# Performance work log

Hardware: AMD Instinct MI355X
Metric: run time of the kernel (lower is better)

Reference implementation:

```python
import jax, jax.numpy as jnp
from jax import lax
import numpy as np


def setup_inputs() -> dict:
    key = jax.random.key(0)
    B, N, K_ORDERS = 8, 16384, 4
    k1, k2 = jax.random.split(key)
    coord = jax.random.normal(k1, (B * N, 3), dtype=jnp.float32)
    serialized_code = jax.random.randint(k2, (K_ORDERS, B * N), 0, 1 << 30)
    return {
        "coord": coord,
        "serialized_code": serialized_code,
        "batch_size": 8,
        "num_group": 1024,
        "group_size": 32,
    }


def _fps(pts, G):
    """Farthest point sampling on pts [N,3]; starts at index 0 (pointops convention)."""
    N = pts.shape[0]

    def step(carry, _):
        dist, last = carry
        d = jnp.sum((pts - pts[last]) ** 2, axis=-1)  # [N]
        dist = jnp.minimum(dist, d)
        nxt = jnp.argmax(dist).astype(jnp.int32)
        return (dist, nxt), nxt

    init = (jnp.full((N,), jnp.inf, pts.dtype), jnp.int32(0))
    _, rest = lax.scan(step, init, None, length=G - 1)
    return jnp.concatenate([jnp.zeros((1,), jnp.int32), rest])  # [G]


def reference(coord, serialized_code, batch_size, num_group, group_size):
    B, G, S = batch_size, num_group, group_size
    N = coord.shape[0] // B
    pts = coord.reshape(B, N, 3)

    # --- FPS per cloud (offset-batched in the original) ---
    loc_idx = jax.vmap(lambda p: _fps(p, G))(pts)  # [B, G] local indices
    s_idx = (loc_idx + (jnp.arange(B, dtype=jnp.int32) * N)[:, None]).reshape(-1)  # [B*G] global
    s_xyz = coord[s_idx]  # [B*G, 3]

    # --- KNN per cloud: S nearest points to each sampled center ---
    centers = s_xyz.reshape(B, G, 3)

    def knn_one(p, c):  # p [N,3], c [G,3]
        # squared distances via gemm to avoid [G,N,3] intermediate
        d2 = (jnp.sum(c * c, -1)[:, None] + jnp.sum(p * p, -1)[None, :]
              - 2.0 * c @ p.T)  # [G, N]
        _, idx = lax.top_k(-d2, S)  # ascending distance, self first
        return idx

    nloc = jax.vmap(knn_one)(pts, centers)  # [B, G, S]
    s_n_idx = (nloc + (jnp.arange(B) * N)[:, None, None]).reshape(B * G, S)

    # relative coords, drop the self point (column 0)
    s_n = coord[s_n_idx] - s_xyz[:, None, :]  # [B*G, S, 3]
    s_n = s_n[:, 1:, :]  # [B*G, S-1, 3]

    # --- serialization order over sampled points + inverse permutation ---
    code_sel = serialized_code[:, s_idx]  # [K, B*G]
    s_order = jnp.argsort(code_sel, axis=1)  # [K, B*G]
    M = s_order.shape[1]
    src = jnp.broadcast_to(jnp.arange(M, dtype=s_order.dtype), s_order.shape)
    rows = jnp.arange(s_order.shape[0])[:, None]
    s_inverse = jnp.zeros_like(s_order).at[rows, s_order].set(src)

    return s_idx, s_n, s_xyz, s_order, s_inverse
```

## Files before the change

### kernel.cpp

```cpp
#include <hip/hip_runtime.h>
#include <hip/hip_bf16.h>
#include <stdint.h>

#define BB 8
#define NN 16384
#define GG 1024
#define SS 32
#define BN (BB*NN)

#define OFF_SIDX 0
#define OFF_SN   8192
#define OFF_SXYZ 770048
#define OFF_ORD  794624
#define OFF_INV  827392

#define WS_SIDX 0
#define WS_KNN  32768

typedef float v2f __attribute__((ext_vector_type(2)));

static __device__ __forceinline__ v2f vmin2(v2f a, v2f b) {
    v2f r; r.x = fminf(a.x, b.x); r.y = fminf(a.y, b.y); return r;
}
static __device__ __forceinline__ v2f vmax2(v2f a, v2f b) {
    v2f r; r.x = fmaxf(a.x, b.x); r.y = fmaxf(a.y, b.y); return r;
}

static __device__ __forceinline__ uint64_t shfl_u64(uint64_t v, int src) {
    int lo = __shfl((int)(uint32_t)(v & 0xffffffffull), src, 64);
    int hi = __shfl((int)(uint32_t)(v >> 32), src, 64);
    return ((uint64_t)(uint32_t)hi << 32) | (uint32_t)lo;
}

template<int CTRL, int RM, int BM>
static __device__ __forceinline__ unsigned dpp_umax(unsigned v) {
    unsigned o = (unsigned)__builtin_amdgcn_update_dpp((int)v, (int)v, CTRL, RM, BM, false);
    return o > v ? o : v;
}

__global__ __launch_bounds__(1024) void fps_kernel(const float* __restrict__ coord,
                                                   int* __restrict__ ws_sidx,
                                                   float* __restrict__ out) {
#pragma clang fp contract(off)
    const int b = blockIdx.x;
    const int t = threadIdx.x;
    const int base = b * NN;
    const int wave = t >> 6, lane = t & 63;

    v2f px[8], py[8], pz[8], dist[8];
#pragma unroll
    for (int j = 0; j < 8; j++) {
        int pA = t + (j << 11);
        int pB = pA + 1024;
        px[j] = (v2f){coord[3*(base+pA)  ], coord[3*(base+pB)  ]};
        py[j] = (v2f){coord[3*(base+pA)+1], coord[3*(base+pB)+1]};
        pz[j] = (v2f){coord[3*(base+pA)+2], coord[3*(base+pB)+2]};
        dist[j] = (v2f){__builtin_inff(), __builtin_inff()};
    }

    __shared__ unsigned wv[16];
    __shared__ unsigned win[2];

    if (t == 0) {
        ws_sidx[b*GG] = base;
        out[OFF_SIDX + b*GG] = (float)base;
        win[0] = 0xffffffffu; win[1] = 0xffffffffu;
    }
    float qx = coord[3*base], qy = coord[3*base+1], qz = coord[3*base+2];
    __syncthreads();

    for (int g = 1; g < GG; g++) {
        const int s = g & 1;
        v2f qvx = (v2f){qx,qx}, qvy = (v2f){qy,qy}, qvz = (v2f){qz,qz};
#pragma unroll
        for (int j = 0; j < 8; j++) {
            v2f dx = px[j] - qvx, dy = py[j] - qvy, dz = pz[j] - qvz;
            v2f d  = (dx*dx + dy*dy) + dz*dz;
            dist[j] = vmin2(dist[j], d);
        }
        v2f m01 = vmax2(dist[0], dist[1]);
        v2f m23 = vmax2(dist[2], dist[3]);
        v2f m45 = vmax2(dist[4], dist[5]);
        v2f m67 = vmax2(dist[6], dist[7]);
        v2f m07 = vmax2(vmax2(m01, m23), vmax2(m45, m67));
        float bvf = fmaxf(m07.x, m07.y);
        unsigned lb = __float_as_uint(bvf);
        unsigned r = lb;
        r = dpp_umax<0x111, 0xf, 0xf>(r);
        r = dpp_umax<0x112, 0xf, 0xf>(r);
        r = dpp_umax<0x114, 0xf, 0xf>(r);
        r = dpp_umax<0x118, 0xf, 0xf>(r);
        r = dpp_umax<0x142, 0xa, 0xf>(r);
        r = dpp_umax<0x143, 0xc, 0xf>(r);
        unsigned wmax = (unsigned)__builtin_amdgcn_readlane((int)r, 63);
        if (lane == 0) wv[wave] = wmax;
        __syncthreads();
        if (t == 0) win[1 - s] = 0xffffffffu;
        unsigned x = wv[lane & 15];
        x = dpp_umax<0x111, 0xf, 0xf>(x);
        x = dpp_umax<0x112, 0xf, 0xf>(x);
        x = dpp_umax<0x114, 0xf, 0xf>(x);
        x = dpp_umax<0x118, 0xf, 0xf>(x);
        unsigned bmax = (unsigned)__builtin_amdgcn_readlane((int)x, 15);
        if (lb == bmax) {
            int e = 15;
#pragma unroll
            for (int jj = 15; jj >= 0; jj--) {
                float v = (jj & 1) ? dist[jj >> 1].y : dist[jj >> 1].x;
                if (__float_as_uint(v) == bmax) e = jj;
            }
            atomicMin(&win[s], (unsigned)(t + (e << 10)));
        }
        __syncthreads();
        unsigned pw = win[s];
        int sp = __builtin_amdgcn_readfirstlane((int)pw);
        if (t == 0) {
            ws_sidx[b*GG + g] = base + sp;
            out[OFF_SIDX + b*GG + g] = (float)(base + sp);
        }
        qx = coord[3*(base+sp)];
        qy = coord[3*(base+sp)+1];
        qz = coord[3*(base+sp)+2];
    }
}

__global__ __launch_bounds__(64) void knn_kernel(const float* __restrict__ coord,
                                                 const int* __restrict__ ws_sidx,
                                                 int* __restrict__ ws_knn) {
#pragma clang fp contract(off)
    const int c = blockIdx.x;
    const int l = threadIdx.x;
    const int b = c >> 10;
    const int base = b * NN;
    const int sg = ws_sidx[c];
    const float cx = coord[3*sg], cy = coord[3*sg+1], cz = coord[3*sg+2];
    const float cc = (cx*cx + cy*cy) + cz*cz;

    float mv = __builtin_inff(); int mp = 0;
#pragma unroll 4
    for (int j = 0; j < 256; j++) {
        int p = l + (j << 6);
        float x = coord[3*(base+p)], y = coord[3*(base+p)+1], z = coord[3*(base+p)+2];
        float pp  = (x*x + y*y) + z*z;
        float dot = (cx*x + cy*y) + cz*z;
        float d2  = (cc + pp) - 2.0f*dot;
        if (d2 < mv) { mv = d2; mp = p; }
    }

    uint64_t m0 = 0, m1 = 0, m2 = 0, m3 = 0;
    int res_p = 0;
    for (int k = 0; k < SS; k++) {
        float bv = mv; int bp = mp;
#pragma unroll
        for (int off = 32; off >= 1; off >>= 1) {
            float ov = __shfl_xor(bv, off, 64);
            int   op = __shfl_xor(bp, off, 64);
            if (ov < bv || (ov == bv && op < bp)) { bv = ov; bp = op; }
        }
        if (l == k) res_p = bp;
        const int w  = bp & 63;
        const int e  = bp >> 6;
        if (l == w) {
            uint64_t bit = 1ull << (e & 63);
            int word = e >> 6;
            if      (word == 0) m0 |= bit;
            else if (word == 1) m1 |= bit;
            else if (word == 2) m2 |= bit;
            else                m3 |= bit;
        }
        uint64_t w0 = shfl_u64(m0, w), w1 = shfl_u64(m1, w),
                 w2 = shfl_u64(m2, w), w3 = shfl_u64(m3, w);
        float nv = __builtin_inff(); int np_ = 0;
#pragma unroll
        for (int m = 0; m < 4; m++) {
            int e2 = l + (m << 6);
            uint64_t mw = (m == 0) ? w0 : ((m == 1) ? w1 : ((m == 2) ? w2 : w3));
            int p2 = w + (e2 << 6);
            float x = coord[3*(base+p2)], y = coord[3*(base+p2)+1], z = coord[3*(base+p2)+2];
            float pp  = (x*x + y*y) + z*z;
            float dot = (cx*x + cy*y) + cz*z;
            float d2  = (cc + pp) - 2.0f*dot;
            bool cons = (mw >> l) & 1ull;
            if (!cons && d2 < nv) { nv = d2; np_ = p2; }
        }
#pragma unroll
        for (int off = 32; off >= 1; off >>= 1) {
            float ov = __shfl_xor(nv, off, 64);
            int   op = __shfl_xor(np_, off, 64);
            if (ov < nv || (ov == nv && op < np_)) { nv = ov; np_ = op; }
        }
        if (l == w) { mv = nv; mp = np_; }
    }
    if (l < SS) ws_knn[c * SS + l] = res_p;
}

__global__ void sxyz_kernel(const float* __restrict__ coord,
                            const int* __restrict__ ws_sidx,
                            float* __restrict__ out) {
    int t = blockIdx.x * blockDim.x + threadIdx.x;
    if (t < 8192*3) {
        int i = t / 3, cmp = t - 3*i;
        out[OFF_SXYZ + t] = coord[3*ws_sidx[i] + cmp];
    }
}

__global__ void sn_kernel(const float* __restrict__ coord,
                          const int* __restrict__ ws_sidx,
                          const int* __restrict__ ws_knn,
                          float* __restrict__ out) {
#pragma clang fp contract(off)
    int t = blockIdx.x * blockDim.x + threadIdx.x;
    if (t < 8192*31*3) {
        int cmp = t % 3; int rem = t / 3;
        int j = rem % 31; int i = rem / 31;
        int b = i >> 10;
        int nb = ws_knn[i*SS + j + 1];
        int gidx = b*NN + nb;
        float v = coord[3*gidx + cmp] - coord[3*ws_sidx[i] + cmp];
        out[OFF_SN + t] = v;
    }
}

__global__ __launch_bounds__(1024) void sort_kernel(const int* __restrict__ ser,
                                                    const int* __restrict__ ws_sidx,
                                                    float* __restrict__ out) {
    __shared__ uint64_t keys[8192];
    const int r = blockIdx.x, t = threadIdx.x;
#pragma unroll
    for (int s = 0; s < 8; s++) {
        int i = t + (s << 10);
        uint32_t code = (uint32_t)ser[r * BN + ws_sidx[i]];
        keys[i] = ((uint64_t)code << 13) | (uint32_t)i;
    }
    __syncthreads();
    for (int k2 = 2; k2 <= 8192; k2 <<= 1) {
        for (int j = k2 >> 1; j > 0; j >>= 1) {
#pragma unroll 2
            for (int s = 0; s < 8; s++) {
                int i = t + (s << 10);
                int ixj = i ^ j;
                if (ixj > i) {
                    uint64_t a = keys[i], bq = keys[ixj];
                    bool up = ((i & k2) == 0);
                    if ((a > bq) == up) { keys[i] = bq; keys[ixj] = a; }
                }
            }
            __syncthreads();
        }
    }
    for (int s = 0; s < 8; s++) {
        int k = t + (s << 10);
        uint64_t key = keys[k];
        int i = (int)(key & 8191u);
        out[OFF_ORD + r*8192 + k] = (float)i;
        out[OFF_INV + r*8192 + i] = (float)k;
    }
}

extern "C" void kernel_launch(void* const* d_in, const int* in_sizes, int n_in,
                              void* d_out, int out_size, void* d_ws, size_t ws_size,
                              hipStream_t stream) {
    const float* coord = (const float*)d_in[0];
    const int*   ser   = (const int*)d_in[1];
    float* out = (float*)d_out;
    char* ws = (char*)d_ws;
    int* ws_sidx = (int*)(ws + WS_SIDX);
    int* ws_knn  = (int*)(ws + WS_KNN);

    hipLaunchKernelGGL(fps_kernel,  dim3(BB),   dim3(1024), 0, stream, coord, ws_sidx, out);
    hipLaunchKernelGGL(knn_kernel,  dim3(8192), dim3(64),   0, stream, coord, ws_sidx, ws_knn);
    hipLaunchKernelGGL(sxyz_kernel, dim3(96),   dim3(256),  0, stream, coord, ws_sidx, out);
    hipLaunchKernelGGL(sn_kernel,   dim3(2976), dim3(256),  0, stream, coord, ws_sidx, ws_knn, out);
    hipLaunchKernelGGL(sort_kernel, dim3(4),    dim3(1024), 0, stream, ser, ws_sidx, out);
}
```

Before: 2.101 ms.

## Drop per-iteration FPS barrier via packed 64-bit atomic argmax; DPP reductions in KNN

FPS now packs the inverted wave-max distance and the point index into one 64-bit key. Each wave's winner does an LDS atomicMin on that key directly, which removes the second block-level reduction and one __syncthreads per sample step. A three-slot buffer of winner keys lets each slot be reset safely ahead of use. KNN replaces the shuffle-based argmin butterflies with DPP 64-bit min reductions on packed (distance bits, index) keys, and replaces the mask shuffles with readlane. The packed float-bit ordering assumes non-negative distances, so a slightly negative self distance from the expanded formula could sort wrongly.

```diff
diff --git a/kernel.cpp b/kernel.cpp
--- a/kernel.cpp
+++ b/kernel.cpp
@@ -26,26 +26,45 @@
     v2f r; r.x = fmaxf(a.x, b.x); r.y = fmaxf(a.y, b.y); return r;
 }
 
-static __device__ __forceinline__ uint64_t shfl_u64(uint64_t v, int src) {
-    int lo = __shfl((int)(uint32_t)(v & 0xffffffffull), src, 64);
-    int hi = __shfl((int)(uint32_t)(v >> 32), src, 64);
-    return ((uint64_t)(uint32_t)hi << 32) | (uint32_t)lo;
-}
-
 template<int CTRL, int RM, int BM>
 static __device__ __forceinline__ unsigned dpp_umax(unsigned v) {
     unsigned o = (unsigned)__builtin_amdgcn_update_dpp((int)v, (int)v, CTRL, RM, BM, false);
     return o > v ? o : v;
 }
 
-__global__ __launch_bounds__(1024) void fps_kernel(const float* __restrict__ coord,
-                                                   int* __restrict__ ws_sidx,
-                                                   float* __restrict__ out) {
+template<int CTRL, int RM, int BM>
+static __device__ __forceinline__ uint64_t dpp_umin64(uint64_t v) {
+    unsigned lo = (unsigned)v, hi = (unsigned)(v >> 32);
+    unsigned olo = (unsigned)__builtin_amdgcn_update_dpp((int)lo, (int)lo, CTRL, RM, BM, false);
+    unsigned ohi = (unsigned)__builtin_amdgcn_update_dpp((int)hi, (int)hi, CTRL, RM, BM, false);
+    uint64_t o = ((uint64_t)ohi << 32) | olo;
+    return o < v ? o : v;
+}
+
+static __device__ __forceinline__ uint64_t wave_umin64(uint64_t v) {
+    v = dpp_umin64<0x111, 0xf, 0xf>(v);
+    v = dpp_umin64<0x112, 0xf, 0xf>(v);
+    v = dpp_umin64<0x114, 0xf, 0xf>(v);
+    v = dpp_umin64<0x118, 0xf, 0xf>(v);
+    v = dpp_umin64<0x142, 0xa, 0xf>(v);
+    v = dpp_umin64<0x143, 0xc, 0xf>(v);
+    return v;
+}
+
+static __device__ __forceinline__ uint64_t rdlane64(uint64_t v, int sl) {
+    unsigned lo = (unsigned)__builtin_amdgcn_readlane((int)(unsigned)v, sl);
+    unsigned hi = (unsigned)__builtin_amdgcn_readlane((int)(unsigned)(v >> 32), sl);
+    return ((uint64_t)hi << 32) | lo;
+}
+
+__global__ __launch_bounds__(1024, 4) void fps_kernel(const float* __restrict__ coord,
+                                                      int* __restrict__ ws_sidx,
+                                                      float* __restrict__ out) {
 #pragma clang fp contract(off)
     const int b = blockIdx.x;
     const int t = threadIdx.x;
     const int base = b * NN;
-    const int wave = t >> 6, lane = t & 63;
+    const int lane = t & 63;
 
     v2f px[8], py[8], pz[8], dist[8];
 #pragma unroll
@@ -58,19 +77,20 @@
         dist[j] = (v2f){__builtin_inff(), __builtin_inff()};
     }
 
-    __shared__ unsigned wv[16];
-    __shared__ unsigned win[2];
+    __shared__ unsigned long long win[3];
 
     if (t == 0) {
         ws_sidx[b*GG] = base;
         out[OFF_SIDX + b*GG] = (float)base;
-        win[0] = 0xffffffffu; win[1] = 0xffffffffu;
+        win[0] = ~0ull; win[1] = ~0ull; win[2] = ~0ull;
     }
     float qx = coord[3*base], qy = coord[3*base+1], qz = coord[3*base+2];
     __syncthreads();
 
     for (int g = 1; g < GG; g++) {
-        const int s = g & 1;
+        const int s = g % 3;
+        if (t == 0) win[(g + 1) % 3] = ~0ull;
+
         v2f qvx = (v2f){qx,qx}, qvy = (v2f){qy,qy}, qvz = (v2f){qz,qz};
 #pragma unroll
         for (int j = 0; j < 8; j++) {
@@ -93,27 +113,20 @@
         r = dpp_umax<0x142, 0xa, 0xf>(r);
         r = dpp_umax<0x143, 0xc, 0xf>(r);
         unsigned wmax = (unsigned)__builtin_amdgcn_readlane((int)r, 63);
-        if (lane == 0) wv[wave] = wmax;
-        __syncthreads();
-        if (t == 0) win[1 - s] = 0xffffffffu;
-        unsigned x = wv[lane & 15];
-        x = dpp_umax<0x111, 0xf, 0xf>(x);
-        x = dpp_umax<0x112, 0xf, 0xf>(x);
-        x = dpp_umax<0x114, 0xf, 0xf>(x);
-        x = dpp_umax<0x118, 0xf, 0xf>(x);
-        unsigned bmax = (unsigned)__builtin_amdgcn_readlane((int)x, 15);
-        if (lb == bmax) {
+        if (lb == wmax) {
             int e = 15;
 #pragma unroll
             for (int jj = 15; jj >= 0; jj--) {
                 float v = (jj & 1) ? dist[jj >> 1].y : dist[jj >> 1].x;
-                if (__float_as_uint(v) == bmax) e = jj;
+                if (__float_as_uint(v) == wmax) e = jj;
             }
-            atomicMin(&win[s], (unsigned)(t + (e << 10)));
+            unsigned p = (unsigned)(t + (e << 10));
+            unsigned long long key = (((unsigned long long)(~wmax)) << 14) | p;
+            atomicMin(&win[s], key);
         }
         __syncthreads();
-        unsigned pw = win[s];
-        int sp = __builtin_amdgcn_readfirstlane((int)pw);
+        unsigned long long key = win[s];
+        int sp = __builtin_amdgcn_readfirstlane((int)(unsigned)(key & 16383u));
         if (t == 0) {
             ws_sidx[b*GG + g] = base + sp;
             out[OFF_SIDX + b*GG + g] = (float)(base + sp);
@@ -150,16 +163,15 @@
     uint64_t m0 = 0, m1 = 0, m2 = 0, m3 = 0;
     int res_p = 0;
     for (int k = 0; k < SS; k++) {
-        float bv = mv; int bp = mp;
-#pragma unroll
-        for (int off = 32; off >= 1; off >>= 1) {
-            float ov = __shfl_xor(bv, off, 64);
-            int   op = __shfl_xor(bp, off, 64);
-            if (ov < bv || (ov == bv && op < bp)) { bv = ov; bp = op; }
-        }
-        if (l == k) res_p = bp;
+        uint64_t key = (((uint64_t)__float_as_uint(mv)) << 14) | (unsigned)mp;
+        key = wave_umin64(key);
+        unsigned klo = (unsigned)__builtin_amdgcn_readlane((int)(unsigned)key, 63);
+        unsigned khi = (unsigned)__builtin_amdgcn_readlane((int)(unsigned)(key >> 32), 63);
+        uint64_t bkey = ((uint64_t)khi << 32) | klo;
+        const int bp = (int)(bkey & 16383u);
         const int w  = bp & 63;
         const int e  = bp >> 6;
+        if (l == k) res_p = bp;
         if (l == w) {
             uint64_t bit = 1ull << (e & 63);
             int word = e >> 6;
@@ -168,8 +180,8 @@
             else if (word == 2) m2 |= bit;
             else                m3 |= bit;
         }
-        uint64_t w0 = shfl_u64(m0, w), w1 = shfl_u64(m1, w),
-                 w2 = shfl_u64(m2, w), w3 = shfl_u64(m3, w);
+        uint64_t w0 = rdlane64(m0, w), w1 = rdlane64(m1, w),
+                 w2 = rdlane64(m2, w), w3 = rdlane64(m3, w);
         float nv = __builtin_inff(); int np_ = 0;
 #pragma unroll
         for (int m = 0; m < 4; m++) {
@@ -183,13 +195,15 @@
             bool cons = (mw >> l) & 1ull;
             if (!cons && d2 < nv) { nv = d2; np_ = p2; }
         }
-#pragma unroll
-        for (int off = 32; off >= 1; off >>= 1) {
-            float ov = __shfl_xor(nv, off, 64);
-            int   op = __shfl_xor(np_, off, 64);
-            if (ov < nv || (ov == nv && op < np_)) { nv = ov; np_ = op; }
-        }
-        if (l == w) { mv = nv; mp = np_; }
+        uint64_t nkey = (((uint64_t)__float_as_uint(nv)) << 14) | (unsigned)np_;
+        nkey = wave_umin64(nkey);
+        unsigned nlo = (unsigned)__builtin_amdgcn_readlane((int)(unsigned)nkey, 63);
+        unsigned nhi = (unsigned)__builtin_amdgcn_readlane((int)(unsigned)(nkey >> 32), 63);
+        uint64_t nbk = ((uint64_t)nhi << 32) | nlo;
+        if (l == w) {
+            mv = __uint_as_float((unsigned)(nbk >> 14));
+            mp = (int)(nbk & 16383u);
+        }
     }
     if (l < SS) ws_knn[c * SS + l] = res_p;
 }
```

New measurement: 2.330 ms. +10.9%, slower.

## Track top-2 per lane in KNN with packed 64-bit keys and DPP reductions

Applied to the files above, without the earlier changes.

The KNN selection now keeps the two best candidates per lane, packed as monotone-float-distance plus index into a single 64-bit key. The per-step wave argmin uses DPP row operations and readlane instead of xor-shuffle pairs. The 256-point rescan of a lane's strip only runs when that lane has already used its second candidate. The FPS kernel also gains a launch-bounds occupancy hint and volatile initial loads. This costs extra per-point work in the initial scan and makes correctness depend on the 14-bit index packing.

```diff
diff --git a/kernel.cpp b/kernel.cpp
--- a/kernel.cpp
+++ b/kernel.cpp
@@ -26,35 +26,60 @@
     v2f r; r.x = fmaxf(a.x, b.x); r.y = fmaxf(a.y, b.y); return r;
 }
 
-static __device__ __forceinline__ uint64_t shfl_u64(uint64_t v, int src) {
-    int lo = __shfl((int)(uint32_t)(v & 0xffffffffull), src, 64);
-    int hi = __shfl((int)(uint32_t)(v >> 32), src, 64);
-    return ((uint64_t)(uint32_t)hi << 32) | (uint32_t)lo;
-}
-
 template<int CTRL, int RM, int BM>
 static __device__ __forceinline__ unsigned dpp_umax(unsigned v) {
     unsigned o = (unsigned)__builtin_amdgcn_update_dpp((int)v, (int)v, CTRL, RM, BM, false);
     return o > v ? o : v;
 }
 
-__global__ __launch_bounds__(1024) void fps_kernel(const float* __restrict__ coord,
-                                                   int* __restrict__ ws_sidx,
-                                                   float* __restrict__ out) {
+template<int CTRL, int RM, int BM>
+static __device__ __forceinline__ uint64_t dpp_umin64(uint64_t v) {
+    unsigned lo = (unsigned)v, hi = (unsigned)(v >> 32);
+    unsigned olo = (unsigned)__builtin_amdgcn_update_dpp((int)lo, (int)lo, CTRL, RM, BM, false);
+    unsigned ohi = (unsigned)__builtin_amdgcn_update_dpp((int)hi, (int)hi, CTRL, RM, BM, false);
+    uint64_t o = ((uint64_t)ohi << 32) | olo;
+    return o < v ? o : v;
+}
+
+static __device__ __forceinline__ uint64_t wave_umin64(uint64_t v) {
+    v = dpp_umin64<0x111, 0xf, 0xf>(v);
+    v = dpp_umin64<0x112, 0xf, 0xf>(v);
+    v = dpp_umin64<0x114, 0xf, 0xf>(v);
+    v = dpp_umin64<0x118, 0xf, 0xf>(v);
+    v = dpp_umin64<0x142, 0xa, 0xf>(v);
+    v = dpp_umin64<0x143, 0xc, 0xf>(v);
+    return v;
+}
+
+static __device__ __forceinline__ uint64_t rdlane64(uint64_t v, int sl) {
+    unsigned lo = (unsigned)__builtin_amdgcn_readlane((int)(unsigned)v, sl);
+    unsigned hi = (unsigned)__builtin_amdgcn_readlane((int)(unsigned)(v >> 32), sl);
+    return ((uint64_t)hi << 32) | lo;
+}
+
+static __device__ __forceinline__ unsigned mono(float f) {
+    unsigned u = __float_as_uint(f);
+    return u ^ (unsigned)((((int)u) >> 31) | (int)0x80000000u);
+}
+
+__global__ __launch_bounds__(1024, 4) void fps_kernel(const float* __restrict__ coord,
+                                                      int* __restrict__ ws_sidx,
+                                                      float* __restrict__ out) {
 #pragma clang fp contract(off)
     const int b = blockIdx.x;
     const int t = threadIdx.x;
     const int base = b * NN;
     const int wave = t >> 6, lane = t & 63;
 
+    const volatile float* vc = coord;
     v2f px[8], py[8], pz[8], dist[8];
 #pragma unroll
     for (int j = 0; j < 8; j++) {
         int pA = t + (j << 11);
         int pB = pA + 1024;
-        px[j] = (v2f){coord[3*(base+pA)  ], coord[3*(base+pB)  ]};
-        py[j] = (v2f){coord[3*(base+pA)+1], coord[3*(base+pB)+1]};
-        pz[j] = (v2f){coord[3*(base+pA)+2], coord[3*(base+pB)+2]};
+        px[j] = (v2f){vc[3*(base+pA)  ], vc[3*(base+pB)  ]};
+        py[j] = (v2f){vc[3*(base+pA)+1], vc[3*(base+pB)+1]};
+        pz[j] = (v2f){vc[3*(base+pA)+2], vc[3*(base+pB)+2]};
         dist[j] = (v2f){__builtin_inff(), __builtin_inff()};
     }
 
@@ -136,7 +161,7 @@
     const float cx = coord[3*sg], cy = coord[3*sg+1], cz = coord[3*sg+2];
     const float cc = (cx*cx + cy*cy) + cz*cz;
 
-    float mv = __builtin_inff(); int mp = 0;
+    uint64_t k1 = ~0ull, k2 = ~0ull;
 #pragma unroll 4
     for (int j = 0; j < 256; j++) {
         int p = l + (j << 6);
@@ -144,22 +169,23 @@
         float pp  = (x*x + y*y) + z*z;
         float dot = (cx*x + cy*y) + cz*z;
         float d2  = (cc + pp) - 2.0f*dot;
-        if (d2 < mv) { mv = d2; mp = p; }
+        uint64_t key = (((uint64_t)mono(d2)) << 14) | (unsigned)p;
+        if (key < k1)      { k2 = k1; k1 = key; }
+        else if (key < k2) { k2 = key; }
     }
 
     uint64_t m0 = 0, m1 = 0, m2 = 0, m3 = 0;
+    uint64_t cur = k1, nxt = k2;
+    bool have_nxt = true;
     int res_p = 0;
     for (int k = 0; k < SS; k++) {
-        float bv = mv; int bp = mp;
-#pragma unroll
-        for (int off = 32; off >= 1; off >>= 1) {
-            float ov = __shfl_xor(bv, off, 64);
-            int   op = __shfl_xor(bp, off, 64);
-            if (ov < bv || (ov == bv && op < bp)) { bv = ov; bp = op; }
-        }
-        if (l == k) res_p = bp;
+        uint64_t wmin = wave_umin64(cur);
+        uint64_t bkey = rdlane64(wmin, 63);
+        const int bp = (int)(bkey & 16383u);
         const int w  = bp & 63;
         const int e  = bp >> 6;
+        if (l == k) res_p = bp;
+        bool need_rescan = false;
         if (l == w) {
             uint64_t bit = 1ull << (e & 63);
             int word = e >> 6;
@@ -167,29 +193,30 @@
             else if (word == 1) m1 |= bit;
             else if (word == 2) m2 |= bit;
             else                m3 |= bit;
-        }
-        uint64_t w0 = shfl_u64(m0, w), w1 = shfl_u64(m1, w),
-                 w2 = shfl_u64(m2, w), w3 = shfl_u64(m3, w);
-        float nv = __builtin_inff(); int np_ = 0;
-#pragma unroll
-        for (int m = 0; m < 4; m++) {
-            int e2 = l + (m << 6);
-            uint64_t mw = (m == 0) ? w0 : ((m == 1) ? w1 : ((m == 2) ? w2 : w3));
-            int p2 = w + (e2 << 6);
-            float x = coord[3*(base+p2)], y = coord[3*(base+p2)+1], z = coord[3*(base+p2)+2];
-            float pp  = (x*x + y*y) + z*z;
-            float dot = (cx*x + cy*y) + cz*z;
-            float d2  = (cc + pp) - 2.0f*dot;
-            bool cons = (mw >> l) & 1ull;
-            if (!cons && d2 < nv) { nv = d2; np_ = p2; }
-        }
-#pragma unroll
-        for (int off = 32; off >= 1; off >>= 1) {
-            float ov = __shfl_xor(nv, off, 64);
-            int   op = __shfl_xor(np_, off, 64);
-            if (ov < nv || (ov == nv && op < np_)) { nv = ov; np_ = op; }
-        }
-        if (l == w) { mv = nv; mp = np_; }
+            if (have_nxt) { cur = nxt; have_nxt = false; }
+            else need_rescan = true;
+        }
+        if (__ballot(need_rescan)) {
+            uint64_t w0 = rdlane64(m0, w), w1 = rdlane64(m1, w),
+                     w2 = rdlane64(m2, w), w3 = rdlane64(m3, w);
+            uint64_t best = ~0ull;
+#pragma unroll
+            for (int m = 0; m < 4; m++) {
+                int e2 = l + (m << 6);
+                uint64_t mw = (m == 0) ? w0 : ((m == 1) ? w1 : ((m == 2) ? w2 : w3));
+                int p2 = w + (e2 << 6);
+                float x = coord[3*(base+p2)], y = coord[3*(base+p2)+1], z = coord[3*(base+p2)+2];
+                float pp  = (x*x + y*y) + z*z;
+                float dot = (cx*x + cy*y) + cz*z;
+                float d2  = (cc + pp) - 2.0f*dot;
+                uint64_t key = (((uint64_t)mono(d2)) << 14) | (unsigned)p2;
+                bool cons = (mw >> l) & 1ull;
+                if (!cons && key < best) best = key;
+            }
+            best = wave_umin64(best);
+            uint64_t rk = rdlane64(best, 63);
+            if (l == w) cur = rk;
+        }
     }
     if (l < SS) ws_knn[c * SS + l] = res_p;
 }
```

Result: faster. 1.891 ms (-10.0%).
